# Optimization experiments

Measured on AMD Instinct MI355X. Metric: run time of the kernel, lower is better.

Reference implementation:

```python
import jax, jax.numpy as jnp
import numpy as np

H, D = 8, 8            # heads, per-head dim (hid_dim = 64)
HID = H * D
L = 6                  # HGTConv layers
NI, NV = 32768, 131072 # num 'instr' / 'var' nodes (batch_size == NI)
E_VV, E_VI, E_IV = 1048576, 524288, 524288
INV_SQRT_D = float(1.0 / np.sqrt(D))


def _seg_softmax(logits, seg, n):
    # softmax over edges grouped by destination node (PyG softmax semantics)
    m = jax.ops.segment_max(logits, seg, num_segments=n)
    m = jnp.where(jnp.isfinite(m), m, 0.0)
    e = jnp.exp(logits - m[seg])
    s = jax.ops.segment_sum(e, seg, num_segments=n)
    return e / (s[seg] + 1e-16)


def _edge_msg(k_src, v_src, q_dst, arel, mrel, prel, src, dst, n_dst):
    # relation-specific transforms: [N_src,H,D] x [H,D,D] -> [N_src,H,D]
    k_rel = jnp.einsum('nhd,hde->nhe', k_src, arel)
    v_rel = jnp.einsum('nhd,hde->nhe', v_src, mrel)
    alpha = jnp.einsum('ehd,ehd->eh', q_dst[dst], k_rel[src]) * prel * INV_SQRT_D  # [E,H]
    w = _seg_softmax(alpha, dst, n_dst)
    return jax.ops.segment_sum(v_rel[src] * w[:, :, None], dst, num_segments=n_dst)


def _kqv(x, Wk, Wq, Wv, bk, bq, bv, n):
    k = (x @ Wk.T + bk).reshape(n, H, D)
    q = (x @ Wq.T + bq).reshape(n, H, D)
    v = (x @ Wv.T + bv).reshape(n, H, D)
    return k, q, v


def _forward(x_instr, x_var,
             Wk_i, Wq_i, Wv_i, Wa_i, bk_i, bq_i, bv_i, ba_i, skip_i,
             Wk_v, Wq_v, Wv_v, Wa_v, bk_v, bq_v, bv_v, ba_v, skip_v,
             arel_vv, mrel_vv, prel_vv, arel_vi, mrel_vi, prel_vi,
             arel_iv, mrel_iv, prel_iv,
             Wqkv, bqkv, Wo, bo,
             mw0, mb0, mw1, mb1, mw2, mb2, mw3, mb3, mw4, mb4, mw5, mb5,
             src_vv, dst_vv, src_vi, dst_vi, src_iv, dst_iv):
    xi, xv = x_instr, x_var
    outs = []
    for l in range(L):
        k_i, q_i, v_i = _kqv(xi, Wk_i[l], Wq_i[l], Wv_i[l], bk_i[l], bq_i[l], bv_i[l], NI)
        k_v, q_v, v_v = _kqv(xv, Wk_v[l], Wq_v[l], Wv_v[l], bk_v[l], bq_v[l], bv_v[l], NV)
        # per-edge-type attention softmax + scatter-sum, then sum over edge types (group='sum')
        agg_v = (_edge_msg(k_v, v_v, q_v, arel_vv[l], mrel_vv[l], prel_vv[l], src_vv, dst_vv, NV)
                 + _edge_msg(k_i, v_i, q_v, arel_iv[l], mrel_iv[l], prel_iv[l], src_iv, dst_iv, NV))
        agg_i = _edge_msg(k_v, v_v, q_i, arel_vi[l], mrel_vi[l], prel_vi[l], src_vi, dst_vi, NI)
        o_i = jax.nn.gelu(agg_i.reshape(NI, HID), approximate=False) @ Wa_i[l].T + ba_i[l]
        b_i = jax.nn.sigmoid(skip_i[l])
        xi = b_i * o_i + (1.0 - b_i) * xi
        o_v = jax.nn.gelu(agg_v.reshape(NV, HID), approximate=False) @ Wa_v[l].T + ba_v[l]
        b_v = jax.nn.sigmoid(skip_v[l])
        xv = b_v * o_v + (1.0 - b_v) * xv
        if l > 0:
            outs.append(xi)
    # jumping-knowledge MultiheadAttention over the L-1 stacked layer outputs
    x = jnp.stack(outs)                        # [S, NI, HID], S = L-1 = 5
    S = x.shape[0]
    qkv = x @ Wqkv.T + bqkv                    # [S, NI, 3*HID]
    q, k, v = jnp.split(qkv, 3, axis=-1)
    q = q.reshape(S, NI, H, D)
    k = k.reshape(S, NI, H, D)
    v = v.reshape(S, NI, H, D)
    sc = jnp.einsum('snhd,tnhd->nhst', q, k) * INV_SQRT_D
    w = jax.nn.softmax(sc, axis=-1)
    o = jnp.einsum('nhst,tnhd->snhd', w, v).reshape(S, NI, HID)
    o = o @ Wo.T + bo
    out = o.sum(axis=0)                        # [NI, HID]; batch_size == NI so view is identity
    for W, b in ((mw0, mb0), (mw1, mb1), (mw2, mb2), (mw3, mb3), (mw4, mb4)):
        out = jax.nn.gelu(out @ W.T + b, approximate=False)
    out = out @ mw5.T + mb5                    # [NI, 1]
    return out[:, 0]


def setup_inputs() -> dict:
    key = jax.random.key(0)
    ks = iter(jax.random.split(key, 64))
    def nrm(shape, scale=1.0):
        return jax.random.normal(next(ks), shape, dtype=jnp.float32) * scale
    d = {}
    d['x_instr'] = nrm((NI, HID))
    d['x_var'] = nrm((NV, HID))
    for t in ('i', 'v'):
        for p in ('Wk', 'Wq', 'Wv', 'Wa'):
            d[f'{p}_{t}'] = nrm((L, HID, HID), (2.0 / HID) ** 0.5)
        for p in ('bk', 'bq', 'bv', 'ba'):
            d[f'{p}_{t}'] = jnp.zeros((L, HID), jnp.float32)
        d[f'skip_{t}'] = jnp.ones((L,), jnp.float32)
    for e in ('vv', 'vi', 'iv'):
        d[f'arel_{e}'] = nrm((L, H, D, D), (1.0 / D) ** 0.5)
        d[f'mrel_{e}'] = nrm((L, H, D, D), (1.0 / D) ** 0.5)
        d[f'prel_{e}'] = jnp.ones((L, H), jnp.float32)
    d['Wqkv'] = nrm((3 * HID, HID), (2.0 / HID) ** 0.5)
    d['bqkv'] = jnp.zeros((3 * HID,), jnp.float32)
    d['Wo'] = nrm((HID, HID), (2.0 / HID) ** 0.5)
    d['bo'] = jnp.zeros((HID,), jnp.float32)
    dims = [64, 32, 16, 8, 4, 2, 1]
    for i in range(6):
        d[f'mw{i}'] = nrm((dims[i + 1], dims[i]), (2.0 / dims[i]) ** 0.5)
        d[f'mb{i}'] = jnp.zeros((dims[i + 1],), jnp.float32)
    d['src_vv'] = jax.random.randint(next(ks), (E_VV,), 0, NV, dtype=jnp.int32).astype(jnp.int64)
    d['dst_vv'] = jax.random.randint(next(ks), (E_VV,), 0, NV, dtype=jnp.int32).astype(jnp.int64)
    d['src_vi'] = jax.random.randint(next(ks), (E_VI,), 0, NV, dtype=jnp.int32).astype(jnp.int64)
    d['dst_vi'] = jax.random.randint(next(ks), (E_VI,), 0, NI, dtype=jnp.int32).astype(jnp.int64)
    d['src_iv'] = jax.random.randint(next(ks), (E_IV,), 0, NI, dtype=jnp.int32).astype(jnp.int64)
    d['dst_iv'] = jax.random.randint(next(ks), (E_IV,), 0, NV, dtype=jnp.int32).astype(jnp.int64)
    return d


def reference(x_instr, x_var,
              Wk_i, Wq_i, Wv_i, Wa_i, bk_i, bq_i, bv_i, ba_i, skip_i,
              Wk_v, Wq_v, Wv_v, Wa_v, bk_v, bq_v, bv_v, ba_v, skip_v,
              arel_vv, mrel_vv, prel_vv, arel_vi, mrel_vi, prel_vi,
              arel_iv, mrel_iv, prel_iv,
              Wqkv, bqkv, Wo, bo,
              mw0, mb0, mw1, mb1, mw2, mb2, mw3, mb3, mw4, mb4, mw5, mb5,
              src_vv, dst_vv, src_vi, dst_vi, src_iv, dst_iv):
    return _forward(x_instr, x_var,
                    Wk_i, Wq_i, Wv_i, Wa_i, bk_i, bq_i, bv_i, ba_i, skip_i,
                    Wk_v, Wq_v, Wv_v, Wa_v, bk_v, bq_v, bv_v, ba_v, skip_v,
                    arel_vv, mrel_vv, prel_vv, arel_vi, mrel_vi, prel_vi,
                    arel_iv, mrel_iv, prel_iv,
                    Wqkv, bqkv, Wo, bo,
                    mw0, mb0, mw1, mb1, mw2, mb2, mw3, mb3, mw4, mb4, mw5, mb5,
                    src_vv, dst_vv, src_vi, dst_vi, src_iv, dst_iv)
```

## Files before the change

kernel.cpp:

```cpp
#include <hip/hip_runtime.h>
#include <cmath>

typedef _Float16 f16_t;
typedef __attribute__((ext_vector_type(8))) short short8;
typedef __attribute__((ext_vector_type(8))) _Float16 half8;
typedef __attribute__((ext_vector_type(4))) float f32x4;
typedef _Float16 h2v __attribute__((ext_vector_type(2)));
typedef _Float16 h8 __attribute__((ext_vector_type(8)));
typedef float f2 __attribute__((ext_vector_type(2)));

#define NI_N 32768
#define NV_N 131072
#define E_VV 1048576
#define E_VI 524288
#define E_IV 524288
#define NT_N (NV_N+NV_N+NI_N)
#define ET_N (E_VV+E_IV+E_VI)
#define SC_WIN 4
#define LOG2E 1.4426950408889634f
#define CHV 192
#define CHI 64
#define CHQ 256

__device__ __forceinline__ float gelu_f(float x){ return 0.5f*x*(1.0f+erff(x*0.7071067811865476f)); }

__device__ __forceinline__ void splitf16(float v, short& hi, short& lo){
  f16_t h=(f16_t)v;
  hi=__builtin_bit_cast(short,h);
  f16_t l=(f16_t)(v-(float)h);
  lo=__builtin_bit_cast(short,l);
}
__device__ __forceinline__ f32x4 mfma16(short8 a, short8 b, f32x4 c){
  return __builtin_amdgcn_mfma_f32_16x16x32_f16(__builtin_bit_cast(half8,a),__builtin_bit_cast(half8,b),c,0,0,0);
}
__device__ __forceinline__ float fexp2(float x){
#if __has_builtin(__builtin_amdgcn_exp2f)
  return __builtin_amdgcn_exp2f(x);
#else
  return exp2f(x);
#endif
}
__device__ __forceinline__ float ldval(const float* p){ return *p; }
__device__ __forceinline__ float ldval(const f16_t* p){ return (float)*p; }
__device__ __forceinline__ void stval(float* p,float v){ *p=v; }
__device__ __forceinline__ void stval(f16_t* p,float v){ *p=(f16_t)v; }

__global__ __launch_bounds__(256) void k_hist3(const int* __restrict__ dvv,const int* __restrict__ div_,
    const int* __restrict__ dvi,int* __restrict__ cnt){
  int i=blockIdx.x*256+threadIdx.x;
  if(i<E_VV) atomicAdd(&cnt[dvv[i]],1);
  else if(i<E_VV+E_IV) atomicAdd(&cnt[NV_N+div_[i-E_VV]],1);
  else atomicAdd(&cnt[2*NV_N+dvi[i-E_VV-E_IV]],1);
}
__global__ __launch_bounds__(512) void k_scan1(const int* __restrict__ cnt,int N,int* __restrict__ rp,int* __restrict__ bsum){
  __shared__ int sh[512];
  int i=blockIdx.x*512+threadIdx.x;
  int v=(i<N)?cnt[i]:0;
  sh[threadIdx.x]=v; __syncthreads();
  for(int off=1;off<512;off<<=1){
    int t=(threadIdx.x>=(unsigned)off)?sh[threadIdx.x-off]:0; __syncthreads();
    sh[threadIdx.x]+=t; __syncthreads();
  }
  if(i<N) rp[i]=sh[threadIdx.x]-v;
  if(threadIdx.x==511) bsum[blockIdx.x]=sh[511];
}
__global__ __launch_bounds__(1024) void k_scan2(const int* __restrict__ bsum,int* __restrict__ boff,int nb){
  __shared__ int sh[1024];
  int t=threadIdx.x;
  int v=(t<nb)?bsum[t]:0;
  sh[t]=v; __syncthreads();
  for(int off=1;off<1024;off<<=1){
    int x=(t>=(unsigned)off)?sh[t-off]:0; __syncthreads();
    sh[t]+=x; __syncthreads();
  }
  if(t<nb) boff[t]=sh[t]-v;
  if(t==1023) boff[nb]=sh[1023];
}
__global__ __launch_bounds__(512) void k_scan3(int* __restrict__ rp,const int* __restrict__ boff,int* __restrict__ cur,int N,int nb){
  int i=blockIdx.x*512+threadIdx.x;
  if(i<N){ int v=rp[i]+boff[i>>9]; rp[i]=v; cur[i]=v; }
  if(i==0) rp[N]=boff[nb];
}
__global__ __launch_bounds__(256) void k_scatter3w(const int* __restrict__ svv,const int* __restrict__ dvv,
    const int* __restrict__ siv,const int* __restrict__ div_,
    const int* __restrict__ svi,const int* __restrict__ dvi,
    int* __restrict__ cur,int* __restrict__ esrc,int dlo,int dhi){
  int i=blockIdx.x*256+threadIdx.x;
  int d,s;
  if(i<E_VV){ d=dvv[i]; if(d<dlo||d>=dhi) return; s=svv[i]*320; }
  else if(i<E_VV+E_IV){ int j=i-E_VV; d=NV_N+div_[j]; if(d<dlo||d>=dhi) return; s=siv[j]*192; }
  else { int j=i-E_VV-E_IV; d=2*NV_N+dvi[j]; if(d<dlo||d>=dhi) return; s=svi[j]*320; }
  int p=atomicAdd(&cur[d],1); esrc[p]=s;
}

__global__ __launch_bounds__(256) void k_castx(const float* __restrict__ xi_in,const float* __restrict__ xv_in,
    f16_t* __restrict__ xi,f16_t* __restrict__ xv){
  int i=blockIdx.x*256+threadIdx.x;
  if(i<NI_N*64) xi[i]=(f16_t)xi_in[i];
  else { int j=i-NI_N*64; xv[j]=(f16_t)xv_in[j]; }
}

struct FoldArgs{
  const float *Wk_i,*Wq_i,*Wv_i,*bk_i,*bq_i,*bv_i;
  const float *Wk_v,*Wq_v,*Wv_v,*bk_v,*bq_v,*bv_v;
  const float *arel_vv,*mrel_vv,*prel_vv,*arel_vi,*mrel_vi,*prel_vi,*arel_iv,*mrel_iv,*prel_iv;
  const float *Wa_i,*Wa_v;
  short *fwh_var,*fwl_var,*fwh_ins,*fwl_ins,*wah_i,*wal_i,*wah_v,*wal_v;
  float *fwb_var,*fwb_ins;
};
__global__ __launch_bounds__(256) void k_fold6(FoldArgs fa){
  int gid=blockIdx.x*256+threadIdx.x;
  if(gid>=6*640*64) return;
  int l=gid/(640*64);
  int rem=gid-l*640*64;
  int r=rem>>6, c=rem&63;
  if(r>=512){
    int ro=r&63;
    const float* W=(r<576)?fa.Wa_i:fa.Wa_v;
    short *sh=((r<576)?fa.wah_i:fa.wah_v)+l*4096, *sl=((r<576)?fa.wal_i:fa.wal_v)+l*4096;
    short h,lo; splitf16(W[l*4096+ro*64+c],h,lo);
    sh[ro*64+c]=h; sl[ro*64+c]=lo;
    return;
  }
  const float *W,*B,*rel=nullptr,*prl=nullptr;
  short *sh,*sl; float *fwb; int orow; bool isq=false;
  if(r<320){
    sh=fa.fwh_var+l*320*64; sl=fa.fwl_var+l*320*64; fwb=fa.fwb_var+l*320; orow=r;
    if(r<64){ W=fa.Wq_v; B=fa.bq_v; isq=true; }
    else if(r<128){ W=fa.Wk_v; B=fa.bk_v; rel=fa.arel_vv; prl=fa.prel_vv; }
    else if(r<192){ W=fa.Wv_v; B=fa.bv_v; rel=fa.mrel_vv; }
    else if(r<256){ W=fa.Wk_v; B=fa.bk_v; rel=fa.arel_vi; prl=fa.prel_vi; }
    else         { W=fa.Wv_v; B=fa.bv_v; rel=fa.mrel_vi; }
  }else{
    int rr=r-320; sh=fa.fwh_ins+l*192*64; sl=fa.fwl_ins+l*192*64; fwb=fa.fwb_ins+l*192; orow=rr;
    if(rr<64){ W=fa.Wq_i; B=fa.bq_i; isq=true; }
    else if(rr<128){ W=fa.Wk_i; B=fa.bk_i; rel=fa.arel_iv; prl=fa.prel_iv; }
    else           { W=fa.Wv_i; B=fa.bv_i; rel=fa.mrel_iv; }
  }
  int d=orow&63;
  float val,bval;
  if(!rel){
    val=W[l*4096+d*64+c]; bval=B[l*64+d];
  }else{
    int h=d>>3, e=d&7;
    float s=prl?prl[l*8+h]*0.3535533905932738f:1.0f;
    float acc=0.f,bacc=0.f;
    #pragma unroll
    for(int dd=0;dd<8;dd++){
      float rv=rel[l*512+h*64+dd*8+e];
      acc += W[l*4096+(h*8+dd)*64+c]*rv;
      bacc+= B[l*64+h*8+dd]*rv;
    }
    val=acc*s; bval=bacc*s;
  }
  if(isq){ val*=LOG2E; bval*=LOG2E; }
  short h2q,lo2; splitf16(val,h2q,lo2);
  sh[orow*64+c]=h2q; sl[orow*64+c]=lo2;
  if(c==0) fwb[orow]=bval;
}

__global__ __launch_bounds__(256) void k_split2(const float* __restrict__ W,int n,short* __restrict__ hi,short* __restrict__ lo){
  int i=blockIdx.x*256+threadIdx.x;
  if(i<n){ short h,l2; splitf16(W[i],h,l2); hi[i]=h; lo[i]=l2; }
}

__device__ __forceinline__ void colres_body(const f16_t* __restrict__ A,int nrb,
    const short* __restrict__ Bh,const short* __restrict__ Bl,
    const float* __restrict__ bias,f16_t* __restrict__ out,int octot,int ocol0,
    int c,int CH,int wave,int lane,int m,int quad,f16_t (*rep)[72])
{
  short8 bhi[4][2], blo[4][2]; float bb[4];
  #pragma unroll
  for(int ot=0;ot<4;ot++){
    size_t o=(size_t)(ocol0+ot*16+m)*64+quad*8;
    bhi[ot][0]=*(const short8*)(Bh+o);    bhi[ot][1]=*(const short8*)(Bh+o+32);
    blo[ot][0]=*(const short8*)(Bl+o);    blo[ot][1]=*(const short8*)(Bl+o+32);
    bb[ot]=bias[ocol0+ot*16+m];
  }
  int rr0=lane>>3, seg=lane&7;
  for(int rb=c;rb<nrb;rb+=CH){
    int row0=rb*64+wave*16;
    const f16_t* ap=A+(size_t)(row0+m)*64+quad*8;
    short8 a0=*(const short8*)(const void*)ap;
    short8 a1=*(const short8*)(const void*)(ap+32);
    f32x4 acc[4];
    #pragma unroll
    for(int ot=0;ot<4;ot++){ f32x4 t={bb[ot],bb[ot],bb[ot],bb[ot]}; acc[ot]=t; }
    #pragma unroll
    for(int ot=0;ot<4;ot++){
      acc[ot]=mfma16(a0,blo[ot][0],acc[ot]);
      acc[ot]=mfma16(a0,bhi[ot][0],acc[ot]);
      acc[ot]=mfma16(a1,blo[ot][1],acc[ot]);
      acc[ot]=mfma16(a1,bhi[ot][1],acc[ot]);
    }
    #pragma unroll
    for(int ot=0;ot<4;ot++)
      #pragma unroll
      for(int r=0;r<4;r++)
        rep[quad*4+r][ot*16+m]=(f16_t)acc[ot][r];
    #pragma unroll
    for(int it=0;it<2;it++){
      int rr=it*8+rr0;
      h8 vals=*(const h8*)&rep[rr][seg*8];
      *(h8*)(out+(size_t)(row0+rr)*octot+ocol0+seg*8)=vals;
    }
  }
}

__global__ __launch_bounds__(256) void k_colres_feat(const f16_t* __restrict__ Av,const f16_t* __restrict__ Ai,
    const short* __restrict__ Bvh,const short* __restrict__ Bvl,const float* __restrict__ biasv,
    const short* __restrict__ Bih,const short* __restrict__ Bil,const float* __restrict__ biasi,
    f16_t* __restrict__ outv,f16_t* __restrict__ outi)
{
  __shared__ f16_t rep[4][16][72];
  const int wave=threadIdx.x>>6, lane=threadIdx.x&63;
  const int m=lane&15, quad=lane>>4;
  int bx=blockIdx.x;
  if(bx<5*CHV){
    int pan=bx/CHV, c=bx%CHV;
    colres_body(Av,NV_N/64,Bvh,Bvl,biasv,outv,320,pan*64,c,CHV,wave,lane,m,quad,rep[wave]);
  }else{
    bx-=5*CHV;
    int pan=bx/CHI, c=bx%CHI;
    colres_body(Ai,NI_N/64,Bih,Bil,biasi,outi,192,pan*64,c,CHI,wave,lane,m,quad,rep[wave]);
  }
}

__global__ __launch_bounds__(256) void k_colres1(const f16_t* __restrict__ A,int nrb,
    const short* __restrict__ Bh,const short* __restrict__ Bl,
    const float* __restrict__ bias,f16_t* __restrict__ out,int octot,int CH)
{
  __shared__ f16_t rep[4][16][72];
  const int wave=threadIdx.x>>6, lane=threadIdx.x&63;
  const int m=lane&15, quad=lane>>4;
  int pan=blockIdx.x/CH, c=blockIdx.x%CH;
  colres_body(A,nrb,Bh,Bl,bias,out,octot,pan*64,c,CH,wave,lane,m,quad,rep[wave]);
}

template<typename AT, typename OT>
__device__ __forceinline__ void gemm_body(const AT* __restrict__ A,int row0,
    const short* __restrict__ Bh,const short* __restrict__ Bl,
    const float* __restrict__ bias,float bias_scale,
    OT* __restrict__ out,int octot,int ocol0,int npanels,int m,int quad,int lane,
    f16_t (*rep)[72])
{
  const AT* ap=A+(size_t)(row0+m)*64+quad*8;
  constexpr bool AF16 = (sizeof(AT)==2);
  short8 ahi[2], alo[2];
  if constexpr(AF16){
    #pragma unroll
    for(int kf=0;kf<2;kf++) ahi[kf]=*(const short8*)(const void*)(ap+kf*32);
  }else{
    #pragma unroll
    for(int kf=0;kf<2;kf++){
      short8 th,tl;
      #pragma unroll
      for(int j=0;j<8;j++){ short h,l2; splitf16(ldval(&ap[kf*32+j]),h,l2); th[j]=h; tl[j]=l2; }
      ahi[kf]=th; alo[kf]=tl;
    }
  }
  for(int pan=0;pan<npanels;pan++){
    int colbase=pan*64;
    short8 bhi[4][2], blo[4][2];
    #pragma unroll
    for(int ot=0;ot<4;ot++){
      size_t o=(size_t)(colbase+ot*16+m)*64+quad*8;
      #pragma unroll
      for(int kf=0;kf<2;kf++){
        bhi[ot][kf]=*(const short8*)(Bh+o+kf*32);
        blo[ot][kf]=*(const short8*)(Bl+o+kf*32);
      }
    }
    f32x4 acc[4];
    #pragma unroll
    for(int ot=0;ot<4;ot++){
      float bv=bias[colbase+ot*16+m]*bias_scale;
      acc[ot][0]=bv; acc[ot][1]=bv; acc[ot][2]=bv; acc[ot][3]=bv;
    }
    #pragma unroll
    for(int ot=0;ot<4;ot++){
      #pragma unroll
      for(int kf=0;kf<2;kf++){
        if constexpr(!AF16) acc[ot]=mfma16(alo[kf],bhi[ot][kf],acc[ot]);
        acc[ot]=mfma16(ahi[kf],blo[ot][kf],acc[ot]);
        acc[ot]=mfma16(ahi[kf],bhi[ot][kf],acc[ot]);
      }
    }
    if constexpr(sizeof(OT)==2){
      #pragma unroll
      for(int ot=0;ot<4;ot++)
        #pragma unroll
        for(int r=0;r<4;r++)
          rep[quad*4+r][ot*16+m]=(f16_t)acc[ot][r];
      #pragma unroll
      for(int it=0;it<2;it++){
        int rr=it*8+(lane>>3), seg=lane&7;
        h8 vals=*(const h8*)&rep[rr][seg*8];
        *(h8*)(out+(size_t)(row0+rr)*octot+ocol0+colbase+seg*8)=vals;
      }
    }else{
      #pragma unroll
      for(int ot=0;ot<4;ot++){
        int col=ocol0+colbase+ot*16+m;
        #pragma unroll
        for(int r=0;r<4;r++){
          int row=row0+quad*4+r;
          stval(&out[(size_t)row*octot+col],acc[ot][r]);
        }
      }
    }
  }
}

template<typename AT, typename OT>
__global__ __launch_bounds__(256) void k_gemm64p(const AT* __restrict__ A,int N,
    const short* __restrict__ Bh,const short* __restrict__ Bl,
    const float* __restrict__ bias,float bias_scale,
    OT* __restrict__ out,int octot,int ocol0,int npanels)
{
  __shared__ f16_t rep[4][16][72];
  const int wave=threadIdx.x>>6, lane=threadIdx.x&63;
  const int m=lane&15, quad=lane>>4;
  const int row0=blockIdx.x*64+wave*16;
  if(row0>=N) return;
  gemm_body<AT,OT>(A,row0,Bh,Bl,bias,bias_scale,out,octot,ocol0,npanels,m,quad,lane,rep[wave]);
}

__global__ __launch_bounds__(256) void k_update2(const f16_t* __restrict__ agg_i,const f16_t* __restrict__ agg_v,
    const short* __restrict__ wah_i,const short* __restrict__ wal_i,
    const short* __restrict__ wah_v,const short* __restrict__ wal_v,
    const float* __restrict__ ba_i,const float* __restrict__ ba_v,
    const float* __restrict__ skip_i,const float* __restrict__ skip_v,
    f16_t* __restrict__ x_i,f16_t* __restrict__ x_v,
    f16_t* __restrict__ outs,int nbi)
{
  __shared__ f16_t rep[4][16][72];
  const int wave=threadIdx.x>>6, lane=threadIdx.x&63;
  const int m=lane&15, quad=lane>>4;
  const bool isI=(int)blockIdx.x<nbi;
  const int row0=(isI?blockIdx.x:(blockIdx.x-nbi))*64+wave*16;
  const f16_t* agg=isI?agg_i:agg_v;
  const short* Wah=isI?wah_i:wah_v;
  const short* Wal=isI?wal_i:wal_v;
  const float* ba=isI?ba_i:ba_v;
  const float* skip=isI?skip_i:skip_v;
  f16_t* x=isI?x_i:x_v;
  f16_t* oo=isI?outs:nullptr;
  f16_t (*R)[72]=rep[wave];
  short8 bhi[4][2], blo[4][2];
  #pragma unroll
  for(int ot=0;ot<4;ot++){
    size_t o=(size_t)(ot*16+m)*64+quad*8;
    #pragma unroll
    for(int kf=0;kf<2;kf++){
      bhi[ot][kf]=*(const short8*)(Wah+o+kf*32);
      blo[ot][kf]=*(const short8*)(Wal+o+kf*32);
    }
  }
  const f16_t* ap=agg+(size_t)(row0+m)*64+quad*8;
  short8 ahi[2], alo[2];
  #pragma unroll
  for(int kf=0;kf<2;kf++){
    short8 th,tl;
    #pragma unroll
    for(int j=0;j<8;j++){ short h,l2; splitf16(gelu_f((float)ap[kf*32+j]),h,l2); th[j]=h; tl[j]=l2; }
    ahi[kf]=th; alo[kf]=tl;
  }
  int rr0=lane>>3, seg=lane&7;
  h8 x0=*(const h8*)(x+(size_t)(row0+rr0)*64+seg*8);
  h8 x1=*(const h8*)(x+(size_t)(row0+8+rr0)*64+seg*8);
  *(h8*)&R[rr0][seg*8]=x0;
  *(h8*)&R[8+rr0][seg*8]=x1;
  f32x4 acc[4];
  #pragma unroll
  for(int ot=0;ot<4;ot++){
    float bv=ba[ot*16+m];
    acc[ot][0]=bv; acc[ot][1]=bv; acc[ot][2]=bv; acc[ot][3]=bv;
  }
  #pragma unroll
  for(int ot=0;ot<4;ot++){
    #pragma unroll
    for(int kf=0;kf<2;kf++){
      acc[ot]=mfma16(alo[kf],bhi[ot][kf],acc[ot]);
      acc[ot]=mfma16(ahi[kf],blo[ot][kf],acc[ot]);
      acc[ot]=mfma16(ahi[kf],bhi[ot][kf],acc[ot]);
    }
  }
  float s=1.0f/(1.0f+__expf(-skip[0]));
  #pragma unroll
  for(int ot=0;ot<4;ot++){
    int col=ot*16+m;
    #pragma unroll
    for(int r=0;r<4;r++){
      int row=quad*4+r;
      float xn=s*acc[ot][r]+(1.0f-s)*(float)R[row][col];
      R[row][col]=(f16_t)xn;
    }
  }
  h8 o0=*(const h8*)&R[rr0][seg*8];
  h8 o1=*(const h8*)&R[8+rr0][seg*8];
  *(h8*)(x+(size_t)(row0+rr0)*64+seg*8)=o0;
  *(h8*)(x+(size_t)(row0+8+rr0)*64+seg*8)=o1;
  if(oo){
    *(h8*)(oo+(size_t)(row0+rr0)*64+seg*8)=o0;
    *(h8*)(oo+(size_t)(row0+8+rr0)*64+seg*8)=o1;
  }
}

__device__ __forceinline__ float edge_agg_eh(const int* __restrict__ rp,const int* __restrict__ es,
    const f16_t* __restrict__ sf,int koff,int voff,int n,int e_slot,int h,int lane,
    h2v q0,h2v q1,h2v q2,h2v q3,float* __restrict__ L)
{
  int b=__builtin_amdgcn_readfirstlane(rp[n]);
  int e=__builtin_amdgcn_readfirstlane(rp[n+1]);
  if(b==e) return 0.f;
  const float M0=-1e30f;
  float m=M0, ls=0.f;
  f2 A0={0.f,0.f},A1={0.f,0.f},A2={0.f,0.f},A3={0.f,0.f};
  const int hb=h*8;
  for(int i=b;i<e;i+=8){
    int eidx=i+e_slot;
    bool valid=eidx<e;
    int ec=valid?eidx:(e-1);
    int off=es[ec];
    const f16_t* kp=sf+(size_t)(unsigned)off+koff+hb;
    h8 kv=*(const h8*)kp;
    h8 vv=*(const h8*)(sf+(size_t)(unsigned)off+voff+hb);
    float p;
#if __has_builtin(__builtin_amdgcn_fdot2)
    p=__builtin_amdgcn_fdot2((h2v){kv[0],kv[1]},q0,0.f,false);
    p=__builtin_amdgcn_fdot2((h2v){kv[2],kv[3]},q1,p,false);
    p=__builtin_amdgcn_fdot2((h2v){kv[4],kv[5]},q2,p,false);
    p=__builtin_amdgcn_fdot2((h2v){kv[6],kv[7]},q3,p,false);
#else
    p=(float)kv[0]*(float)q0[0]+(float)kv[1]*(float)q0[1]
     +(float)kv[2]*(float)q1[0]+(float)kv[3]*(float)q1[1]
     +(float)kv[4]*(float)q2[0]+(float)kv[5]*(float)q2[1]
     +(float)kv[6]*(float)q3[0]+(float)kv[7]*(float)q3[1];
#endif
    p=valid?p:M0;
    float mn=fmaxf(m,p);
    float sc=fexp2(m-mn);
    float w=valid?fexp2(p-mn):0.f;
    ls=fmaf(ls,sc,w);
    f2 S={sc,sc}, W={w,w};
    f2 V0={(float)vv[0],(float)vv[1]}, V1={(float)vv[2],(float)vv[3]};
    f2 V2={(float)vv[4],(float)vv[5]}, V3={(float)vv[6],(float)vv[7]};
    A0=A0*S+W*V0; A1=A1*S+W*V1; A2=A2*S+W*V2; A3=A3*S+W*V3;
    m=mn;
  }
  float mall=fmaxf(m,__shfl_xor(m,8));
  mall=fmaxf(mall,__shfl_xor(mall,16));
  mall=fmaxf(mall,__shfl_xor(mall,32));
  float scl=fexp2(m-mall);
  ls*=scl;
  float lsall=ls+__shfl_xor(ls,8);
  lsall+=__shfl_xor(lsall,16);
  lsall+=__shfl_xor(lsall,32);
  f2 S2={scl,scl};
  A0*=S2; A1*=S2; A2*=S2; A3*=S2;
  float* wp=L+e_slot*64+hb;
  f32x4 w0={A0[0],A0[1],A1[0],A1[1]};
  f32x4 w1={A2[0],A2[1],A3[0],A3[1]};
  *(f32x4*)wp=w0;
  *(f32x4*)(wp+4)=w1;
  __asm__ volatile("s_waitcnt lgkmcnt(0)" ::: "memory");
  float r=0.f;
  #pragma unroll
  for(int ee=0;ee<8;ee++) r+=L[ee*64+lane];
  float lsr=__shfl(lsall,lane>>3);
  return r/(lsr+1e-16f);
}

__global__ __launch_bounds__(256) void k_edge_all(const int* __restrict__ rp_all,const int* __restrict__ es,
    const f16_t* __restrict__ var_feat,const f16_t* __restrict__ ins_feat,
    f16_t* __restrict__ agg_v,f16_t* __restrict__ agg_i,int nbv)
{
  __shared__ float lds[4][512];
  int wave=threadIdx.x>>6, lane=threadIdx.x&63;
  int e_slot=lane>>3, h=lane&7;
  float* L=lds[wave];
  if((int)blockIdx.x<nbv){
    int n=blockIdx.x*4+wave;
    const f16_t* qp=var_feat+(size_t)n*320+h*8;
    h8 qv=*(const h8*)qp;
    h2v q0={qv[0],qv[1]},q1={qv[2],qv[3]},q2={qv[4],qv[5]},q3={qv[6],qv[7]};
    float r1=edge_agg_eh(rp_all,es,var_feat,64,128,n,e_slot,h,lane,q0,q1,q2,q3,L);
    float r2=edge_agg_eh(rp_all+NV_N,es,ins_feat,64,128,n,e_slot,h,lane,q0,q1,q2,q3,L);
    agg_v[(size_t)n*64+lane]=(f16_t)(r1+r2);
  }else{
    int n=(blockIdx.x-nbv)*4+wave;
    const f16_t* qp=ins_feat+(size_t)n*192+h*8;
    h8 qv=*(const h8*)qp;
    h2v q0={qv[0],qv[1]},q1={qv[2],qv[3]},q2={qv[4],qv[5]},q3={qv[6],qv[7]};
    float r=edge_agg_eh(rp_all+2*NV_N,es,var_feat,192,256,n,e_slot,h,lane,q0,q1,q2,q3,L);
    agg_i[(size_t)n*64+lane]=(f16_t)r;
  }
}

__global__ __launch_bounds__(256) void k_jk(const f16_t* __restrict__ qkv,float* __restrict__ osum,int n_nodes){
  int wave=threadIdx.x>>6, lane=threadIdx.x&63;
  int n=blockIdx.x*4+wave;
  if(n>=n_nodes) return;
  float q[5],k[5],v[5];
  #pragma unroll
  for(int s=0;s<5;s++){
    const f16_t* p=qkv+((size_t)s*n_nodes+n)*192;
    q[s]=(float)p[lane]; k[s]=(float)p[64+lane]; v[s]=(float)p[128+lane];
  }
  float sc[5][5];
  #pragma unroll
  for(int s=0;s<5;s++)
    #pragma unroll
    for(int t=0;t<5;t++){
      float x=q[s]*k[t];
      x+=__shfl_xor(x,1); x+=__shfl_xor(x,2); x+=__shfl_xor(x,4);
      sc[s][t]=x*0.3535533905932738f;
    }
  float os=0.f;
  #pragma unroll
  for(int s=0;s<5;s++){
    float m=sc[s][0];
    #pragma unroll
    for(int t=1;t<5;t++) m=fmaxf(m,sc[s][t]);
    float den=0.f, acc=0.f;
    #pragma unroll
    for(int t=0;t<5;t++){ float e=__expf(sc[s][t]-m); den+=e; acc+=e*v[t]; }
    os+=acc/den;
  }
  osum[(size_t)n*64+lane]=os;
}

struct MlpArgs{ const float *w0,*b0,*w1,*b1,*w2,*b2,*w3,*b3,*w4,*b4,*w5,*b5; };
__global__ __launch_bounds__(256) void k_mlp(const float* __restrict__ in,MlpArgs ma,float* __restrict__ out,int N){
  __shared__ float sw0[2048],sb0[32],sw1[512],sb1[16],sw2[128],sb2[8],sw3[32],sb3[4],sw4[8],sb4[2],sw5[2],sb5[1];
  for(int i=threadIdx.x;i<2048;i+=256) sw0[i]=ma.w0[i];
  for(int i=threadIdx.x;i<512;i+=256)  sw1[i]=ma.w1[i];
  if(threadIdx.x<128) sw2[threadIdx.x]=ma.w2[threadIdx.x];
  if(threadIdx.x<32){ sb0[threadIdx.x]=ma.b0[threadIdx.x]; sw3[threadIdx.x]=ma.w3[threadIdx.x]; }
  if(threadIdx.x<16) sb1[threadIdx.x]=ma.b1[threadIdx.x];
  if(threadIdx.x<8){ sb2[threadIdx.x]=ma.b2[threadIdx.x]; sw4[threadIdx.x]=ma.w4[threadIdx.x]; }
  if(threadIdx.x<4) sb3[threadIdx.x]=ma.b3[threadIdx.x];
  if(threadIdx.x<2){ sb4[threadIdx.x]=ma.b4[threadIdx.x]; sw5[threadIdx.x]=ma.w5[threadIdx.x]; }
  if(threadIdx.x==0) sb5[0]=ma.b5[0];
  __syncthreads();
  int n=blockIdx.x*256+threadIdx.x;
  if(n>=N) return;
  float a[64];
  const f32x4* p4=(const f32x4*)(in+(size_t)n*64);
  #pragma unroll
  for(int j=0;j<16;j++){ f32x4 t=p4[j]; a[4*j]=t[0]; a[4*j+1]=t[1]; a[4*j+2]=t[2]; a[4*j+3]=t[3]; }
  float h1[32];
  #pragma unroll
  for(int o=0;o<32;o++){ float s=sb0[o];
    #pragma unroll
    for(int c=0;c<64;c++) s+=a[c]*sw0[o*64+c];
    h1[o]=gelu_f(s); }
  float h2q[16];
  #pragma unroll
  for(int o=0;o<16;o++){ float s=sb1[o];
    #pragma unroll
    for(int c=0;c<32;c++) s+=h1[c]*sw1[o*32+c];
    h2q[o]=gelu_f(s); }
  float h3[8];
  #pragma unroll
  for(int o=0;o<8;o++){ float s=sb2[o];
    #pragma unroll
    for(int c=0;c<16;c++) s+=h2q[c]*sw2[o*16+c];
    h3[o]=gelu_f(s); }
  float h4[4];
  #pragma unroll
  for(int o=0;o<4;o++){ float s=sb3[o];
    #pragma unroll
    for(int c=0;c<8;c++) s+=h3[c]*sw3[o*8+c];
    h4[o]=gelu_f(s); }
  float h5[2];
  #pragma unroll
  for(int o=0;o<2;o++){ float s=sb4[o];
    #pragma unroll
    for(int c=0;c<4;c++) s+=h4[c]*sw4[o*4+c];
    h5[o]=gelu_f(s); }
  float r=sb5[0]+h5[0]*sw5[0]+h5[1]*sw5[1];
  out[n]=r;
}

extern "C" void kernel_launch(void* const* d_in,const int* in_sizes,int n_in,
                              void* d_out,int out_size,void* d_ws,size_t ws_size,
                              hipStream_t stream){
  (void)in_sizes;(void)n_in;(void)out_size;(void)ws_size;
  const float* x_instr=(const float*)d_in[0];
  const float* x_var  =(const float*)d_in[1];
  const float* ba_i=(const float*)d_in[9];
  const float* skip_i=(const float*)d_in[10];
  const float* ba_v=(const float*)d_in[18];
  const float* skip_v=(const float*)d_in[19];
  const float* Wqkv=(const float*)d_in[29];
  const float* bqkv=(const float*)d_in[30];
  const float* Wo=(const float*)d_in[31];
  const float* bo=(const float*)d_in[32];
  const int* src_vv=(const int*)d_in[45];
  const int* dst_vv=(const int*)d_in[46];
  const int* src_vi=(const int*)d_in[47];
  const int* dst_vi=(const int*)d_in[48];
  const int* src_iv=(const int*)d_in[49];
  const int* dst_iv=(const int*)d_in[50];

  char* w=(char*)d_ws;
  auto alloc=[&](size_t b)->char*{ char* p=w; w+=(b+255)&~(size_t)255; return p; };
  int* rp_all=(int*)alloc((size_t)(NT_N+1)*4);
  int* cnt_all=(int*)alloc((size_t)NT_N*4);
  int* cur_all=(int*)alloc((size_t)NT_N*4);
  int* bsum =(int*)alloc(640*4);
  int* boff =(int*)alloc(640*4);
  int* esrc_all=(int*)alloc((size_t)ET_N*4);
  short* fwh_var=(short*)alloc((size_t)6*320*64*2);
  short* fwl_var=(short*)alloc((size_t)6*320*64*2);
  float* fwb_var=(float*)alloc((size_t)6*320*4);
  short* fwh_ins=(short*)alloc((size_t)6*192*64*2);
  short* fwl_ins=(short*)alloc((size_t)6*192*64*2);
  float* fwb_ins=(float*)alloc((size_t)6*192*4);
  short* wah_i=(short*)alloc((size_t)6*64*64*2);
  short* wal_i=(short*)alloc((size_t)6*64*64*2);
  short* wah_v=(short*)alloc((size_t)6*64*64*2);
  short* wal_v=(short*)alloc((size_t)6*64*64*2);
  short* qkvh=(short*)alloc(192*64*2);
  short* qkvl=(short*)alloc(192*64*2);
  short* woh=(short*)alloc(64*64*2);
  short* wol=(short*)alloc(64*64*2);
  f16_t* outs=(f16_t*)alloc((size_t)5*NI_N*64*2);
  char* arena=alloc((size_t)146800640);
  f16_t*  xv      =(f16_t*)(arena);
  f16_t*  xi      =(f16_t*)(arena+16777216);
  f16_t*  var_feat=(f16_t*)(arena+20971520);
  f16_t*  ins_feat=(f16_t*)(arena+104857600);
  f16_t*  agg_v   =(f16_t*)(arena+117440512);
  f16_t*  agg_i   =(f16_t*)(arena+134217728);
  f16_t*  qkv    =(f16_t*)(arena);
  float*  osum   =(float*)(arena+67108864);
  float*  out_jk =(float*)(arena+75497472);

  hipMemsetAsync(cnt_all,0,(size_t)NT_N*4,stream);
  k_hist3<<<ET_N/256,256,0,stream>>>(dst_vv,dst_iv,dst_vi,cnt_all);
  int nb=NT_N/512;
  k_scan1<<<nb,512,0,stream>>>(cnt_all,NT_N,rp_all,bsum);
  k_scan2<<<1,1024,0,stream>>>(bsum,boff,nb);
  k_scan3<<<nb,512,0,stream>>>(rp_all,boff,cur_all,NT_N,nb);
  for(int wdx=0;wdx<SC_WIN;wdx++){
    int dlo=wdx*(NT_N/SC_WIN), dhi=(wdx+1)*(NT_N/SC_WIN);
    k_scatter3w<<<ET_N/256,256,0,stream>>>(src_vv,dst_vv,src_iv,dst_iv,src_vi,dst_vi,cur_all,esrc_all,dlo,dhi);
  }

  k_castx<<<(NI_N*64+NV_N*64)/256,256,0,stream>>>(x_instr,x_var,xi,xv);

  k_split2<<<(192*64+255)/256,256,0,stream>>>(Wqkv,192*64,qkvh,qkvl);
  k_split2<<<(64*64+255)/256,256,0,stream>>>(Wo,64*64,woh,wol);

  FoldArgs fa;
  fa.Wk_i=(const float*)d_in[2]; fa.Wq_i=(const float*)d_in[3]; fa.Wv_i=(const float*)d_in[4];
  fa.bk_i=(const float*)d_in[6]; fa.bq_i=(const float*)d_in[7]; fa.bv_i=(const float*)d_in[8];
  fa.Wk_v=(const float*)d_in[11]; fa.Wq_v=(const float*)d_in[12]; fa.Wv_v=(const float*)d_in[13];
  fa.bk_v=(const float*)d_in[15]; fa.bq_v=(const float*)d_in[16]; fa.bv_v=(const float*)d_in[17];
  fa.arel_vv=(const float*)d_in[20]; fa.mrel_vv=(const float*)d_in[21]; fa.prel_vv=(const float*)d_in[22];
  fa.arel_vi=(const float*)d_in[23]; fa.mrel_vi=(const float*)d_in[24]; fa.prel_vi=(const float*)d_in[25];
  fa.arel_iv=(const float*)d_in[26]; fa.mrel_iv=(const float*)d_in[27]; fa.prel_iv=(const float*)d_in[28];
  fa.Wa_i=(const float*)d_in[5]; fa.Wa_v=(const float*)d_in[14];
  fa.fwh_var=fwh_var; fa.fwl_var=fwl_var; fa.fwh_ins=fwh_ins; fa.fwl_ins=fwl_ins;
  fa.wah_i=wah_i; fa.wal_i=wal_i; fa.wah_v=wah_v; fa.wal_v=wal_v;
  fa.fwb_var=fwb_var; fa.fwb_ins=fwb_ins;
  k_fold6<<<(6*640*64)/256,256,0,stream>>>(fa);

  for(int l=0;l<6;l++){
    k_colres_feat<<<5*CHV+3*CHI,256,0,stream>>>(xv,xi,
        fwh_var+(size_t)l*320*64,fwl_var+(size_t)l*320*64,fwb_var+l*320,
        fwh_ins+(size_t)l*192*64,fwl_ins+(size_t)l*192*64,fwb_ins+l*192,
        var_feat,ins_feat);
    k_edge_all<<<NV_N/4+NI_N/4,256,0,stream>>>(rp_all,esrc_all,var_feat,ins_feat,agg_v,agg_i,NV_N/4);
    k_update2<<<NI_N/64+NV_N/64,256,0,stream>>>(agg_i,agg_v,
        wah_i+(size_t)l*4096,wal_i+(size_t)l*4096,wah_v+(size_t)l*4096,wal_v+(size_t)l*4096,
        ba_i+l*64,ba_v+l*64,skip_i+l,skip_v+l,xi,xv,
        (l>0)?(outs+(size_t)(l-1)*NI_N*64):nullptr,NI_N/64);
  }

  k_colres1<<<3*CHQ,256,0,stream>>>(outs,5*NI_N/64,qkvh,qkvl,bqkv,qkv,192,CHQ);
  k_jk<<<NI_N/4,256,0,stream>>>(qkv,osum,NI_N);
  k_gemm64p<float,float><<<NI_N/64,256,0,stream>>>(osum,NI_N,woh,wol,bo,5.0f,out_jk,64,0,1);
  MlpArgs ma;
  ma.w0=(const float*)d_in[33]; ma.b0=(const float*)d_in[34];
  ma.w1=(const float*)d_in[35]; ma.b1=(const float*)d_in[36];
  ma.w2=(const float*)d_in[37]; ma.b2=(const float*)d_in[38];
  ma.w3=(const float*)d_in[39]; ma.b3=(const float*)d_in[40];
  ma.w4=(const float*)d_in[41]; ma.b4=(const float*)d_in[42];
  ma.w5=(const float*)d_in[43]; ma.b5=(const float*)d_in[44];
  k_mlp<<<NI_N/256,256,0,stream>>>(out_jk,ma,(float*)d_out,NI_N);
}
```

Before: 1.529 ms.

## Software-pipeline edge gathers, process 16 edges per step, interleave edge types

```diff
diff --git a/kernel.cpp b/kernel.cpp
--- a/kernel.cpp
+++ b/kernel.cpp
@@ -21,6 +21,7 @@
 #define CHV 192
 #define CHI 64
 #define CHQ 256
+#define EPAD 68
 
 __device__ __forceinline__ float gelu_f(float x){ return 0.5f*x*(1.0f+erff(x*0.7071067811865476f)); }
 
@@ -407,93 +408,153 @@
   }
 }
 
-__device__ __forceinline__ float edge_agg_eh(const int* __restrict__ rp,const int* __restrict__ es,
-    const f16_t* __restrict__ sf,int koff,int voff,int n,int e_slot,int h,int lane,
-    h2v q0,h2v q1,h2v q2,h2v q3,float* __restrict__ L)
-{
-  int b=__builtin_amdgcn_readfirstlane(rp[n]);
-  int e=__builtin_amdgcn_readfirstlane(rp[n+1]);
-  if(b==e) return 0.f;
-  const float M0=-1e30f;
-  float m=M0, ls=0.f;
-  f2 A0={0.f,0.f},A1={0.f,0.f},A2={0.f,0.f},A3={0.f,0.f};
-  const int hb=h*8;
-  for(int i=b;i<e;i+=8){
-    int eidx=i+e_slot;
-    bool valid=eidx<e;
-    int ec=valid?eidx:(e-1);
-    int off=es[ec];
-    const f16_t* kp=sf+(size_t)(unsigned)off+koff+hb;
-    h8 kv=*(const h8*)kp;
-    h8 vv=*(const h8*)(sf+(size_t)(unsigned)off+voff+hb);
-    float p;
+struct ELoad { h8 ka,va,kb,vb; };
+struct EState { float m, ls; f2 A0,A1,A2,A3; };
+
+__device__ __forceinline__ void einit(EState& S){
+  S.m=-1e30f; S.ls=0.f;
+  f2 z={0.f,0.f};
+  S.A0=z; S.A1=z; S.A2=z; S.A3=z;
+}
+
+__device__ __forceinline__ ELoad eload16(const int* __restrict__ es,int i,int e,
+    int e_slot,const f16_t* __restrict__ sfh)
+{
+  int em1=e-1;
+  int ia=i+e_slot, ib=ia+8;
+  int ca=ia<em1?ia:em1;
+  int cb=ib<em1?ib:em1;
+  int oa=es[ca], ob=es[cb];
+  const f16_t* pa=sfh+(unsigned)oa;
+  const f16_t* pb=sfh+(unsigned)ob;
+  ELoad L;
+  L.ka=*(const h8*)pa;
+  L.va=*(const h8*)(pa+64);
+  L.kb=*(const h8*)pb;
+  L.vb=*(const h8*)(pb+64);
+  return L;
+}
+
+__device__ __forceinline__ float dot8(h8 k,h2v q0,h2v q1,h2v q2,h2v q3){
 #if __has_builtin(__builtin_amdgcn_fdot2)
-    p=__builtin_amdgcn_fdot2((h2v){kv[0],kv[1]},q0,0.f,false);
-    p=__builtin_amdgcn_fdot2((h2v){kv[2],kv[3]},q1,p,false);
-    p=__builtin_amdgcn_fdot2((h2v){kv[4],kv[5]},q2,p,false);
-    p=__builtin_amdgcn_fdot2((h2v){kv[6],kv[7]},q3,p,false);
+  float p=__builtin_amdgcn_fdot2((h2v){k[0],k[1]},q0,0.f,false);
+  p=__builtin_amdgcn_fdot2((h2v){k[2],k[3]},q1,p,false);
+  p=__builtin_amdgcn_fdot2((h2v){k[4],k[5]},q2,p,false);
+  p=__builtin_amdgcn_fdot2((h2v){k[6],k[7]},q3,p,false);
+  return p;
 #else
-    p=(float)kv[0]*(float)q0[0]+(float)kv[1]*(float)q0[1]
-     +(float)kv[2]*(float)q1[0]+(float)kv[3]*(float)q1[1]
-     +(float)kv[4]*(float)q2[0]+(float)kv[5]*(float)q2[1]
-     +(float)kv[6]*(float)q3[0]+(float)kv[7]*(float)q3[1];
+  return (float)k[0]*(float)q0[0]+(float)k[1]*(float)q0[1]
+        +(float)k[2]*(float)q1[0]+(float)k[3]*(float)q1[1]
+        +(float)k[4]*(float)q2[0]+(float)k[5]*(float)q2[1]
+        +(float)k[6]*(float)q3[0]+(float)k[7]*(float)q3[1];
 #endif
-    p=valid?p:M0;
-    float mn=fmaxf(m,p);
-    float sc=fexp2(m-mn);
-    float w=valid?fexp2(p-mn):0.f;
-    ls=fmaf(ls,sc,w);
-    f2 S={sc,sc}, W={w,w};
-    f2 V0={(float)vv[0],(float)vv[1]}, V1={(float)vv[2],(float)vv[3]};
-    f2 V2={(float)vv[4],(float)vv[5]}, V3={(float)vv[6],(float)vv[7]};
-    A0=A0*S+W*V0; A1=A1*S+W*V1; A2=A2*S+W*V2; A3=A3*S+W*V3;
-    m=mn;
-  }
-  float mall=fmaxf(m,__shfl_xor(m,8));
+}
+
+__device__ __forceinline__ void ecompute16(const ELoad& L,int i,int e,int e_slot,
+    h2v q0,h2v q1,h2v q2,h2v q3,EState& S)
+{
+  float pa=dot8(L.ka,q0,q1,q2,q3);
+  float pb=dot8(L.kb,q0,q1,q2,q3);
+  float mn=fmaxf(S.m,fmaxf(pa,pb));
+  float sc=fexp2(S.m-mn);
+  bool oka=(i+e_slot)<e, okb=(i+e_slot+8)<e;
+  float wa=oka?fexp2(pa-mn):0.f;
+  float wb=okb?fexp2(pb-mn):0.f;
+  S.ls=fmaf(S.ls,sc,wa+wb);
+  f2 SS={sc,sc}, WA={wa,wa}, WB={wb,wb};
+  S.A0=S.A0*SS+WA*(f2){(float)L.va[0],(float)L.va[1]}+WB*(f2){(float)L.vb[0],(float)L.vb[1]};
+  S.A1=S.A1*SS+WA*(f2){(float)L.va[2],(float)L.va[3]}+WB*(f2){(float)L.vb[2],(float)L.vb[3]};
+  S.A2=S.A2*SS+WA*(f2){(float)L.va[4],(float)L.va[5]}+WB*(f2){(float)L.vb[4],(float)L.vb[5]};
+  S.A3=S.A3*SS+WA*(f2){(float)L.va[6],(float)L.va[7]}+WB*(f2){(float)L.vb[6],(float)L.vb[7]};
+  S.m=mn;
+}
+
+__device__ __forceinline__ void efinish(EState& S){
+  float mall=fmaxf(S.m,__shfl_xor(S.m,8));
   mall=fmaxf(mall,__shfl_xor(mall,16));
   mall=fmaxf(mall,__shfl_xor(mall,32));
-  float scl=fexp2(m-mall);
-  ls*=scl;
+  float scl=fexp2(S.m-mall);
+  float ls=S.ls*scl;
   float lsall=ls+__shfl_xor(ls,8);
   lsall+=__shfl_xor(lsall,16);
   lsall+=__shfl_xor(lsall,32);
-  f2 S2={scl,scl};
-  A0*=S2; A1*=S2; A2*=S2; A3*=S2;
-  float* wp=L+e_slot*64+hb;
-  f32x4 w0={A0[0],A0[1],A1[0],A1[1]};
-  f32x4 w1={A2[0],A2[1],A3[0],A3[1]};
-  *(f32x4*)wp=w0;
-  *(f32x4*)(wp+4)=w1;
-  __asm__ volatile("s_waitcnt lgkmcnt(0)" ::: "memory");
-  float r=0.f;
-  #pragma unroll
-  for(int ee=0;ee<8;ee++) r+=L[ee*64+lane];
-  float lsr=__shfl(lsall,lane>>3);
-  return r/(lsr+1e-16f);
+  float nrm=scl/(lsall+1e-16f);
+  f2 N={nrm,nrm};
+  S.A0*=N; S.A1*=N; S.A2*=N; S.A3*=N;
 }
 
 __global__ __launch_bounds__(256) void k_edge_all(const int* __restrict__ rp_all,const int* __restrict__ es,
     const f16_t* __restrict__ var_feat,const f16_t* __restrict__ ins_feat,
     f16_t* __restrict__ agg_v,f16_t* __restrict__ agg_i,int nbv)
 {
-  __shared__ float lds[4][512];
+  __shared__ float lds[4][8*EPAD];
   int wave=threadIdx.x>>6, lane=threadIdx.x&63;
-  int e_slot=lane>>3, h=lane&7;
+  int e_slot=lane>>3, h=lane&7, hb=h*8;
   float* L=lds[wave];
   if((int)blockIdx.x<nbv){
     int n=blockIdx.x*4+wave;
-    const f16_t* qp=var_feat+(size_t)n*320+h*8;
-    h8 qv=*(const h8*)qp;
+    int b1=__builtin_amdgcn_readfirstlane(rp_all[n]);
+    int e1=__builtin_amdgcn_readfirstlane(rp_all[n+1]);
+    const int* rp2=rp_all+NV_N;
+    int b2=__builtin_amdgcn_readfirstlane(rp2[n]);
+    int e2=__builtin_amdgcn_readfirstlane(rp2[n+1]);
+    h8 qv=*(const h8*)(var_feat+(size_t)n*320+hb);
     h2v q0={qv[0],qv[1]},q1={qv[2],qv[3]},q2={qv[4],qv[5]},q3={qv[6],qv[7]};
-    float r1=edge_agg_eh(rp_all,es,var_feat,64,128,n,e_slot,h,lane,q0,q1,q2,q3,L);
-    float r2=edge_agg_eh(rp_all+NV_N,es,ins_feat,64,128,n,e_slot,h,lane,q0,q1,q2,q3,L);
-    agg_v[(size_t)n*64+lane]=(f16_t)(r1+r2);
+    const f16_t* sfh1=var_feat+64+hb;
+    const f16_t* sfh2=ins_feat+64+hb;
+    EState S1,S2; einit(S1); einit(S2);
+    int i1=b1,i2=b2;
+    bool a1=b1<e1, a2=b2<e2;
+    ELoad L1,L2;
+    if(a1) L1=eload16(es,i1,e1,e_slot,sfh1);
+    if(a2) L2=eload16(es,i2,e2,e_slot,sfh2);
+    while(a1||a2){
+      if(a1){
+        ecompute16(L1,i1,e1,e_slot,q0,q1,q2,q3,S1);
+        i1+=16; a1=i1<e1;
+        if(a1) L1=eload16(es,i1,e1,e_slot,sfh1);
+      }
+      if(a2){
+        ecompute16(L2,i2,e2,e_slot,q0,q1,q2,q3,S2);
+        i2+=16; a2=i2<e2;
+        if(a2) L2=eload16(es,i2,e2,e_slot,sfh2);
+      }
+    }
+    efinish(S1); efinish(S2);
+    f2 W0=S1.A0+S2.A0, W1=S1.A1+S2.A1, W2=S1.A2+S2.A2, W3=S1.A3+S2.A3;
+    float* wp=L+e_slot*EPAD+hb;
+    *(f32x4*)wp=(f32x4){W0[0],W0[1],W1[0],W1[1]};
+    *(f32x4*)(wp+4)=(f32x4){W2[0],W2[1],W3[0],W3[1]};
+    __asm__ volatile("s_waitcnt lgkmcnt(0)" ::: "memory");
+    float r=0.f;
+    #pragma unroll
+    for(int ee=0;ee<8;ee++) r+=L[ee*EPAD+lane];
+    agg_v[(size_t)n*64+lane]=(f16_t)r;
   }else{
     int n=(blockIdx.x-nbv)*4+wave;
-    const f16_t* qp=ins_feat+(size_t)n*192+h*8;
-    h8 qv=*(const h8*)qp;
+    const int* rp=rp_all+2*NV_N;
+    int b=__builtin_amdgcn_readfirstlane(rp[n]);
+    int e=__builtin_amdgcn_readfirstlane(rp[n+1]);
+    h8 qv=*(const h8*)(ins_feat+(size_t)n*192+hb);
     h2v q0={qv[0],qv[1]},q1={qv[2],qv[3]},q2={qv[4],qv[5]},q3={qv[6],qv[7]};
-    float r=edge_agg_eh(rp_all+2*NV_N,es,var_feat,192,256,n,e_slot,h,lane,q0,q1,q2,q3,L);
+    const f16_t* sfh=var_feat+192+hb;
+    EState S; einit(S);
+    int i=b; bool a=b<e;
+    ELoad Ld;
+    if(a) Ld=eload16(es,i,e,e_slot,sfh);
+    while(a){
+      ecompute16(Ld,i,e,e_slot,q0,q1,q2,q3,S);
+      i+=16; a=i<e;
+      if(a) Ld=eload16(es,i,e,e_slot,sfh);
+    }
+    efinish(S);
+    float* wp=L+e_slot*EPAD+hb;
+    *(f32x4*)wp=(f32x4){S.A0[0],S.A0[1],S.A1[0],S.A1[1]};
+    *(f32x4*)(wp+4)=(f32x4){S.A2[0],S.A2[1],S.A3[0],S.A3[1]};
+    __asm__ volatile("s_waitcnt lgkmcnt(0)" ::: "memory");
+    float r=0.f;
+    #pragma unroll
+    for(int ee=0;ee<8;ee++) r+=L[ee*EPAD+lane];
     agg_i[(size_t)n*64+lane]=(f16_t)r;
   }
 }
```

Measured after the change: 1.610 ms. 1.05x slower.
